# Performance work log

Hardware: AMD Instinct MI355X
Metric: run time of the kernel (lower is better)

Reference implementation:

```python
import jax, jax.numpy as jnp
import numpy as np

EPS = 1e-6


def _att_vector(x, W, b, sharp2, th2, is_last):
    """AttentionVector on a 2D payoff slice.
    x: (N, a, m). W: (1, 2), b: (1,). Returns (N, a)."""
    # compare_param: pair (x[n,j,k], x[n,i,k]) -> Linear(2,1) -> sigmoid -> mean over k
    # Linear on the concat pair is w00*x[n,j,k] + w01*x[n,i,k] + b, so we fuse it.
    lin = W[0, 0] * x[:, None, :, :] + W[0, 1] * x[:, :, None, :] + b[0]  # (N,a,a,m)
    c = jnp.mean(jax.nn.sigmoid(lin), axis=3)  # (N,a,a)
    # max_normalize over dim 2
    c = c / (jnp.max(c, axis=2, keepdims=True) + EPS)
    # compute_player_mask
    m = jnp.mean(c, axis=2)  # (N,a)
    m = jax.nn.relu(m * sharp2[0] + th2[0])
    m = jax.nn.softmax(m, axis=1)
    if not is_last:
        m = m / (jnp.max(m, axis=1, keepdims=True) + EPS)
    return m


def setup_inputs() -> dict:
    key = jax.random.key(0)
    ks = jax.random.split(key, 16)
    N, a1, a2, f = 128, 64, 64, 2
    inp = {
        "x": jax.random.normal(ks[0], (N, f, a1, a2), dtype=jnp.float32),
        "fc_W": jax.random.normal(ks[1], (2, 2), dtype=jnp.float32) * 0.5,
        "fc_b": jax.random.normal(ks[2], (2,), dtype=jnp.float32) * 0.1,
        "p1_W": jax.random.normal(ks[3], (1, 2), dtype=jnp.float32) * 0.5,
        "p1_b": jax.random.normal(ks[4], (1,), dtype=jnp.float32) * 0.1,
        "p1_sharp": jnp.ones((1,), dtype=jnp.float32),
        "p1_th": jnp.zeros((1,), dtype=jnp.float32),
        "p2_W": jax.random.normal(ks[5], (1, 2), dtype=jnp.float32) * 0.5,
        "p2_b": jax.random.normal(ks[6], (1,), dtype=jnp.float32) * 0.1,
        "p2_sharp": jnp.ones((1,), dtype=jnp.float32),
        "p2_th": jnp.zeros((1,), dtype=jnp.float32),
        "out_W": jax.random.normal(ks[7], (1, 2), dtype=jnp.float32) * 0.5,
        "out_b": jax.random.normal(ks[8], (1,), dtype=jnp.float32) * 0.1,
        "out_sharp": jnp.ones((1,), dtype=jnp.float32),
        "out_th": jnp.zeros((1,), dtype=jnp.float32),
    }
    return inp


def reference(x, fc_W, fc_b, p1_W, p1_b, p1_sharp, p1_th,
              p2_W, p2_b, p2_sharp, p2_th,
              out_W, out_b, out_sharp, out_th):
    # x: (N, f=2, a1, a2) -> (N, a1, a2, f)
    h = jnp.transpose(x, (0, 2, 3, 1))
    # is_fc_first: Linear(2, 2) + ReLU on last dim
    h = jax.nn.relu(h @ fc_W.T + fc_b)  # (N,a1,a2,2)
    # one AttentionModule (module_layers=1, not simult)
    vec1 = _att_vector(h[..., 0], p1_W, p1_b, p1_sharp, p1_th, is_last=False)  # (N,a1)
    h = h * vec1[:, :, None, None]
    pl2 = jnp.transpose(h[..., 1], (0, 2, 1))  # (N,a2,a1)
    vec2 = _att_vector(pl2, p2_W, p2_b, p2_sharp, p2_th, is_last=False)  # (N,a2)
    h = h * vec2[:, None, :, None]
    # with_last: final AttentionVector (is_last=True) on player-1 channel
    out = _att_vector(h[..., 0], out_W, out_b, out_sharp, out_th, is_last=True)  # (N,a1)
    return out
```

## Files before the change

kernel.cpp:

```cpp
#include <hip/hip_runtime.h>


constexpr int A   = 64;
constexpr int PAD = 65;
constexpr float L2E  = 1.4426950408889634f;
constexpr float EPSF = 1e-6f;

__device__ __forceinline__ float bcast(float v, int srcLane) {
    return __int_as_float(__builtin_amdgcn_readlane(__float_as_int(v), srcLane));
}
__device__ __forceinline__ float rcpf(float v) { return __builtin_amdgcn_rcpf(v); }
__device__ __forceinline__ float ex2(float v)  { return __builtin_amdgcn_exp2f(v); }

__device__ __forceinline__ void att2(const float* __restrict__ prow,
                                     const float* __restrict__ qrow,
                                     int row0, int lane,
                                     float* __restrict__ gm)
{
    float acc0 = 0.f, acc1 = 0.f;
#pragma unroll 1
    for (int c = 0; c < 4; ++c) {
        float pk[16], qk[16];
#pragma unroll
        for (int t = 0; t < 16; ++t) {
            pk[t] = prow[c * 16 + t];
            qk[t] = qrow[c * 16 + t];
        }
#pragma unroll
        for (int t = 0; t < 16; ++t) {
            float q0 = bcast(qk[t], row0);
            float q1 = bcast(qk[t], row0 + 1);
            acc0 += rcpf(fmaf(pk[t], q0, 1.0f));
            acc1 += rcpf(fmaf(pk[t], q1, 1.0f));
        }
    }
    float s0 = acc0, m0 = acc0, s1 = acc1, m1v = acc1;
#pragma unroll
    for (int off = 1; off < 64; off <<= 1) {
        s0 += __shfl_xor(s0, off, 64);
        m0 = fmaxf(m0, __shfl_xor(m0, off, 64));
        s1 += __shfl_xor(s1, off, 64);
        m1v = fmaxf(m1v, __shfl_xor(m1v, off, 64));
    }
    if (lane == 0) {
        gm[row0]     = (s0 * (1.0f / 4096.0f)) / (m0 * (1.0f / 64.0f) + EPSF);
        gm[row0 + 1] = (s1 * (1.0f / 4096.0f)) / (m1v * (1.0f / 64.0f) + EPSF);
    }
}

__device__ __forceinline__ float softmax64(float m, float sharp, float th, bool last)
{
    float v = fmaxf(0.f, m * sharp + th);
    float mx = v;
#pragma unroll
    for (int off = 1; off < 64; off <<= 1) mx = fmaxf(mx, __shfl_xor(mx, off, 64));
    float e = __expf(v - mx);
    float s = e;
#pragma unroll
    for (int off = 1; off < 64; off <<= 1) s += __shfl_xor(s, off, 64);
    float r = e / s;
    if (!last) {
        float rm = r;
#pragma unroll
        for (int off = 1; off < 64; off <<= 1) rm = fmaxf(rm, __shfl_xor(rm, off, 64));
        r = r / (rm + EPSF);
    }
    return r;
}

__global__ __launch_bounds__(1024, 1)
void k_stageB(const float* __restrict__ x,
              const float* __restrict__ fcW, const float* __restrict__ fcb,
              const float* __restrict__ p1W, const float* __restrict__ p1b,
              float* __restrict__ m1)
{
    __shared__ float pL[A * PAD];
    __shared__ float qL[A * PAD];
    const int tid = threadIdx.x, lane = tid & 63, wv = tid >> 6;
    const int n = blockIdx.x >> 1, half = blockIdx.x & 1;

    const float4* x0v = (const float4*)(x + (size_t)n * 2 * A * A);
    const float4* x1v = x0v + (A * A / 4);
    float4 a = x0v[tid];
    float4 c = x1v[tid];
    const float w00 = fcW[0], w01 = fcW[1], b0 = fcb[0];
    const float W0 = p1W[0], W1 = p1W[1], bb = p1b[0];
    const int e = tid * 4, i = e >> 6, j = e & 63;
    float hv[4] = { fmaxf(0.f, w00 * a.x + w01 * c.x + b0),
                    fmaxf(0.f, w00 * a.y + w01 * c.y + b0),
                    fmaxf(0.f, w00 * a.z + w01 * c.z + b0),
                    fmaxf(0.f, w00 * a.w + w01 * c.w + b0) };
#pragma unroll
    for (int t = 0; t < 4; ++t) {
        pL[i * PAD + j + t] = ex2(-L2E * (W0 * hv[t] + bb));
        qL[i * PAD + j + t] = ex2(-L2E * (W1 * hv[t]));
    }
    __syncthreads();

    const int row0 = half * 32 + wv * 2;
    att2(pL + lane * PAD, qL + lane * PAD, row0, lane, m1 + (size_t)n * A);
}

__global__ __launch_bounds__(1024, 1)
void k_stageC(const float* __restrict__ x,
              const float* __restrict__ fcW, const float* __restrict__ fcb,
              const float* __restrict__ p1s, const float* __restrict__ p1t,
              const float* __restrict__ p2W, const float* __restrict__ p2b,
              const float* __restrict__ m1, float* __restrict__ m2)
{
    __shared__ float pL[A * PAD];
    __shared__ float qL[A * PAD];
    __shared__ float v1buf[A];
    const int tid = threadIdx.x, lane = tid & 63, wv = tid >> 6;
    const int n = blockIdx.x >> 1, half = blockIdx.x & 1;

    const float4* x0v = (const float4*)(x + (size_t)n * 2 * A * A);
    const float4* x1v = x0v + (A * A / 4);
    float4 a = x0v[tid];
    float4 c = x1v[tid];

    if (tid < 64) v1buf[tid] = softmax64(m1[(size_t)n * A + tid], p1s[0], p1t[0], false);
    __syncthreads();

    const float w10 = fcW[2], w11 = fcW[3], b1 = fcb[1];
    const float W0 = p2W[0], W1 = p2W[1], bb = p2b[0];
    const int e = tid * 4, i = e >> 6, j = e & 63;
    const float sc = v1buf[i];
    float hv[4] = { fmaxf(0.f, w10 * a.x + w11 * c.x + b1) * sc,
                    fmaxf(0.f, w10 * a.y + w11 * c.y + b1) * sc,
                    fmaxf(0.f, w10 * a.z + w11 * c.z + b1) * sc,
                    fmaxf(0.f, w10 * a.w + w11 * c.w + b1) * sc };
#pragma unroll
    for (int t = 0; t < 4; ++t) {
        pL[(j + t) * PAD + i] = ex2(-L2E * (W0 * hv[t] + bb));
        qL[(j + t) * PAD + i] = ex2(-L2E * (W1 * hv[t]));
    }
    __syncthreads();

    const int row0 = half * 32 + wv * 2;
    att2(pL + lane * PAD, qL + lane * PAD, row0, lane, m2 + (size_t)n * A);
}

__global__ __launch_bounds__(1024, 1)
void k_stageD(const float* __restrict__ x,
              const float* __restrict__ fcW, const float* __restrict__ fcb,
              const float* __restrict__ p1s, const float* __restrict__ p1t,
              const float* __restrict__ p2s, const float* __restrict__ p2t,
              const float* __restrict__ oW,  const float* __restrict__ ob,
              const float* __restrict__ m1,  const float* __restrict__ m2,
              float* __restrict__ m3)
{
    __shared__ float pL[A * PAD];
    __shared__ float qL[A * PAD];
    __shared__ float v1buf[A], v2buf[A];
    const int tid = threadIdx.x, lane = tid & 63, wv = tid >> 6;
    const int n = blockIdx.x >> 1, half = blockIdx.x & 1;

    const float4* x0v = (const float4*)(x + (size_t)n * 2 * A * A);
    const float4* x1v = x0v + (A * A / 4);
    float4 a = x0v[tid];
    float4 c = x1v[tid];

    if (tid < 64)       v1buf[tid]      = softmax64(m1[(size_t)n * A + tid],      p1s[0], p1t[0], false);
    else if (tid < 128) v2buf[tid - 64] = softmax64(m2[(size_t)n * A + tid - 64], p2s[0], p2t[0], false);
    __syncthreads();

    const float w00 = fcW[0], w01 = fcW[1], b0 = fcb[0];
    const float W0 = oW[0], W1 = oW[1], bb = ob[0];
    const int e = tid * 4, i = e >> 6, j = e & 63;
    const float sc = v1buf[i];
    float hv[4] = { fmaxf(0.f, w00 * a.x + w01 * c.x + b0) * sc * v2buf[j],
                    fmaxf(0.f, w00 * a.y + w01 * c.y + b0) * sc * v2buf[j + 1],
                    fmaxf(0.f, w00 * a.z + w01 * c.z + b0) * sc * v2buf[j + 2],
                    fmaxf(0.f, w00 * a.w + w01 * c.w + b0) * sc * v2buf[j + 3] };
#pragma unroll
    for (int t = 0; t < 4; ++t) {
        pL[i * PAD + j + t] = ex2(-L2E * (W0 * hv[t] + bb));
        qL[i * PAD + j + t] = ex2(-L2E * (W1 * hv[t]));
    }
    __syncthreads();

    const int row0 = half * 32 + wv * 2;
    att2(pL + lane * PAD, qL + lane * PAD, row0, lane, m3 + (size_t)n * A);
}

__global__ __launch_bounds__(64, 1)
void k_final(const float* __restrict__ m3,
             const float* __restrict__ os, const float* __restrict__ ot,
             float* __restrict__ out)
{
    const int n = blockIdx.x, lane = threadIdx.x;
    out[(size_t)n * A + lane] = softmax64(m3[(size_t)n * A + lane], os[0], ot[0], true);
}

extern "C" void kernel_launch(void* const* d_in, const int* in_sizes, int n_in,
                              void* d_out, int out_size, void* d_ws, size_t ws_size,
                              hipStream_t stream)
{
    (void)n_in; (void)out_size; (void)ws_size;
    const float* x   = (const float*)d_in[0];
    const float* fcW = (const float*)d_in[1];
    const float* fcb = (const float*)d_in[2];
    const float* p1W = (const float*)d_in[3];
    const float* p1b = (const float*)d_in[4];
    const float* p1s = (const float*)d_in[5];
    const float* p1t = (const float*)d_in[6];
    const float* p2W = (const float*)d_in[7];
    const float* p2b = (const float*)d_in[8];
    const float* p2s = (const float*)d_in[9];
    const float* p2t = (const float*)d_in[10];
    const float* oW  = (const float*)d_in[11];
    const float* ob  = (const float*)d_in[12];
    const float* os  = (const float*)d_in[13];
    const float* ot  = (const float*)d_in[14];
    float* out = (float*)d_out;

    const int N = in_sizes[0] / (2 * A * A);
    float* ws = (float*)d_ws;
    float* m1 = ws;
    float* m2 = ws + (size_t)N * A;
    float* m3 = ws + (size_t)2 * N * A;

    k_stageB<<<2 * N, 1024, 0, stream>>>(x, fcW, fcb, p1W, p1b, m1);
    k_stageC<<<2 * N, 1024, 0, stream>>>(x, fcW, fcb, p1s, p1t, p2W, p2b, m1, m2);
    k_stageD<<<2 * N, 1024, 0, stream>>>(x, fcW, fcb, p1s, p1t, p2s, p2t, oW, ob, m1, m2, m3);
    k_final<<<N, 64, 0, stream>>>(m3, os, ot, out);
}
```

Before: 112.7 us.

## Fuse all attention stages into one per-sample kernel with 4-row accumulation

Replaces the three stage kernels and the final softmax kernel with a single kernel that runs one 1024-thread block per sample. The per-stage row vectors now stay in shared memory instead of a global workspace, and x is loaded once rather than three times. The pairwise sigmoid reduction now processes four rows per wave instead of two, for more instruction-level parallelism. In exchange the grid shrinks from 2N to N blocks, so half as many blocks cover the GPU and each does twice the work. The launch bound of 4 blocks per CU may also force a tight register cap.

```diff
diff --git a/kernel.cpp b/kernel.cpp
--- a/kernel.cpp
+++ b/kernel.cpp
@@ -12,12 +12,11 @@
 __device__ __forceinline__ float rcpf(float v) { return __builtin_amdgcn_rcpf(v); }
 __device__ __forceinline__ float ex2(float v)  { return __builtin_amdgcn_exp2f(v); }
 
-__device__ __forceinline__ void att2(const float* __restrict__ prow,
+__device__ __forceinline__ void att4(const float* __restrict__ prow,
                                      const float* __restrict__ qrow,
-                                     int row0, int lane,
-                                     float* __restrict__ gm)
+                                     int row0, int lane, float* __restrict__ mbuf)
 {
-    float acc0 = 0.f, acc1 = 0.f;
+    float acc0 = 0.f, acc1 = 0.f, acc2 = 0.f, acc3 = 0.f;
 #pragma unroll 1
     for (int c = 0; c < 4; ++c) {
         float pk[16], qk[16];
@@ -30,21 +29,28 @@
         for (int t = 0; t < 16; ++t) {
             float q0 = bcast(qk[t], row0);
             float q1 = bcast(qk[t], row0 + 1);
+            float q2 = bcast(qk[t], row0 + 2);
+            float q3 = bcast(qk[t], row0 + 3);
             acc0 += rcpf(fmaf(pk[t], q0, 1.0f));
             acc1 += rcpf(fmaf(pk[t], q1, 1.0f));
+            acc2 += rcpf(fmaf(pk[t], q2, 1.0f));
+            acc3 += rcpf(fmaf(pk[t], q3, 1.0f));
         }
     }
-    float s0 = acc0, m0 = acc0, s1 = acc1, m1v = acc1;
+    float s[4] = {acc0, acc1, acc2, acc3};
+    float m[4] = {acc0, acc1, acc2, acc3};
 #pragma unroll
     for (int off = 1; off < 64; off <<= 1) {
-        s0 += __shfl_xor(s0, off, 64);
-        m0 = fmaxf(m0, __shfl_xor(m0, off, 64));
-        s1 += __shfl_xor(s1, off, 64);
-        m1v = fmaxf(m1v, __shfl_xor(m1v, off, 64));
+#pragma unroll
+        for (int r = 0; r < 4; ++r) {
+            s[r] += __shfl_xor(s[r], off, 64);
+            m[r] = fmaxf(m[r], __shfl_xor(m[r], off, 64));
+        }
     }
     if (lane == 0) {
-        gm[row0]     = (s0 * (1.0f / 4096.0f)) / (m0 * (1.0f / 64.0f) + EPSF);
-        gm[row0 + 1] = (s1 * (1.0f / 4096.0f)) / (m1v * (1.0f / 64.0f) + EPSF);
+#pragma unroll
+        for (int r = 0; r < 4; ++r)
+            mbuf[row0 + r] = (s[r] * (1.0f / 4096.0f)) / (m[r] * (1.0f / 64.0f) + EPSF);
     }
 }
 
@@ -68,136 +74,98 @@
     return r;
 }
 
-__global__ __launch_bounds__(1024, 1)
-void k_stageB(const float* __restrict__ x,
-              const float* __restrict__ fcW, const float* __restrict__ fcb,
-              const float* __restrict__ p1W, const float* __restrict__ p1b,
-              float* __restrict__ m1)
+__global__ __launch_bounds__(1024, 4)
+void attn_fused(const float* __restrict__ x,
+                const float* __restrict__ fcW, const float* __restrict__ fcb,
+                const float* __restrict__ p1W, const float* __restrict__ p1b,
+                const float* __restrict__ p1s, const float* __restrict__ p1t,
+                const float* __restrict__ p2W, const float* __restrict__ p2b,
+                const float* __restrict__ p2s, const float* __restrict__ p2t,
+                const float* __restrict__ oW,  const float* __restrict__ ob,
+                const float* __restrict__ os,  const float* __restrict__ ot,
+                float* __restrict__ out)
 {
     __shared__ float pL[A * PAD];
     __shared__ float qL[A * PAD];
+    __shared__ float mbuf[A];
+    __shared__ float v1buf[A], v2buf[A];
+
     const int tid = threadIdx.x, lane = tid & 63, wv = tid >> 6;
-    const int n = blockIdx.x >> 1, half = blockIdx.x & 1;
+    const int n = blockIdx.x;
+    const int row0 = wv * 4;
+    const int i = tid >> 4, j = (tid & 15) * 4;
 
     const float4* x0v = (const float4*)(x + (size_t)n * 2 * A * A);
     const float4* x1v = x0v + (A * A / 4);
-    float4 a = x0v[tid];
-    float4 c = x1v[tid];
-    const float w00 = fcW[0], w01 = fcW[1], b0 = fcb[0];
-    const float W0 = p1W[0], W1 = p1W[1], bb = p1b[0];
-    const int e = tid * 4, i = e >> 6, j = e & 63;
-    float hv[4] = { fmaxf(0.f, w00 * a.x + w01 * c.x + b0),
-                    fmaxf(0.f, w00 * a.y + w01 * c.y + b0),
-                    fmaxf(0.f, w00 * a.z + w01 * c.z + b0),
-                    fmaxf(0.f, w00 * a.w + w01 * c.w + b0) };
+    const float4 a = x0v[tid];
+    const float4 c = x1v[tid];
+    const float w00 = fcW[0], w01 = fcW[1], w10 = fcW[2], w11 = fcW[3];
+    const float b0 = fcb[0], b1 = fcb[1];
+
+    const float h0v[4] = { fmaxf(0.f, w00 * a.x + w01 * c.x + b0),
+                           fmaxf(0.f, w00 * a.y + w01 * c.y + b0),
+                           fmaxf(0.f, w00 * a.z + w01 * c.z + b0),
+                           fmaxf(0.f, w00 * a.w + w01 * c.w + b0) };
+    const float h1v[4] = { fmaxf(0.f, w10 * a.x + w11 * c.x + b1),
+                           fmaxf(0.f, w10 * a.y + w11 * c.y + b1),
+                           fmaxf(0.f, w10 * a.z + w11 * c.z + b1),
+                           fmaxf(0.f, w10 * a.w + w11 * c.w + b1) };
+
+    {
+        const float W0 = p1W[0], W1 = p1W[1], bb = p1b[0];
 #pragma unroll
-    for (int t = 0; t < 4; ++t) {
-        pL[i * PAD + j + t] = ex2(-L2E * (W0 * hv[t] + bb));
-        qL[i * PAD + j + t] = ex2(-L2E * (W1 * hv[t]));
+        for (int t = 0; t < 4; ++t) {
+            pL[i * PAD + j + t] = ex2(-L2E * (W0 * h0v[t] + bb));
+            qL[i * PAD + j + t] = ex2(-L2E * (W1 * h0v[t]));
+        }
     }
     __syncthreads();
-
-    const int row0 = half * 32 + wv * 2;
-    att2(pL + lane * PAD, qL + lane * PAD, row0, lane, m1 + (size_t)n * A);
-}
-
-__global__ __launch_bounds__(1024, 1)
-void k_stageC(const float* __restrict__ x,
-              const float* __restrict__ fcW, const float* __restrict__ fcb,
-              const float* __restrict__ p1s, const float* __restrict__ p1t,
-              const float* __restrict__ p2W, const float* __restrict__ p2b,
-              const float* __restrict__ m1, float* __restrict__ m2)
-{
-    __shared__ float pL[A * PAD];
-    __shared__ float qL[A * PAD];
-    __shared__ float v1buf[A];
-    const int tid = threadIdx.x, lane = tid & 63, wv = tid >> 6;
-    const int n = blockIdx.x >> 1, half = blockIdx.x & 1;
-
-    const float4* x0v = (const float4*)(x + (size_t)n * 2 * A * A);
-    const float4* x1v = x0v + (A * A / 4);
-    float4 a = x0v[tid];
-    float4 c = x1v[tid];
-
-    if (tid < 64) v1buf[tid] = softmax64(m1[(size_t)n * A + tid], p1s[0], p1t[0], false);
+    att4(pL + lane * PAD, qL + lane * PAD, row0, lane, mbuf);
+    __syncthreads();
+    if (wv == 0) v1buf[lane] = softmax64(mbuf[lane], p1s[0], p1t[0], false);
     __syncthreads();
 
-    const float w10 = fcW[2], w11 = fcW[3], b1 = fcb[1];
-    const float W0 = p2W[0], W1 = p2W[1], bb = p2b[0];
-    const int e = tid * 4, i = e >> 6, j = e & 63;
-    const float sc = v1buf[i];
-    float hv[4] = { fmaxf(0.f, w10 * a.x + w11 * c.x + b1) * sc,
-                    fmaxf(0.f, w10 * a.y + w11 * c.y + b1) * sc,
-                    fmaxf(0.f, w10 * a.z + w11 * c.z + b1) * sc,
-                    fmaxf(0.f, w10 * a.w + w11 * c.w + b1) * sc };
+    {
+        const float W0 = p2W[0], W1 = p2W[1], bb = p2b[0];
+        const float sc = v1buf[i];
 #pragma unroll
-    for (int t = 0; t < 4; ++t) {
-        pL[(j + t) * PAD + i] = ex2(-L2E * (W0 * hv[t] + bb));
-        qL[(j + t) * PAD + i] = ex2(-L2E * (W1 * hv[t]));
+        for (int t = 0; t < 4; ++t) {
+            float hv = h1v[t] * sc;
+            pL[(j + t) * PAD + i] = ex2(-L2E * (W0 * hv + bb));
+            qL[(j + t) * PAD + i] = ex2(-L2E * (W1 * hv));
+        }
     }
     __syncthreads();
-
-    const int row0 = half * 32 + wv * 2;
-    att2(pL + lane * PAD, qL + lane * PAD, row0, lane, m2 + (size_t)n * A);
-}
-
-__global__ __launch_bounds__(1024, 1)
-void k_stageD(const float* __restrict__ x,
-              const float* __restrict__ fcW, const float* __restrict__ fcb,
-              const float* __restrict__ p1s, const float* __restrict__ p1t,
-              const float* __restrict__ p2s, const float* __restrict__ p2t,
-              const float* __restrict__ oW,  const float* __restrict__ ob,
-              const float* __restrict__ m1,  const float* __restrict__ m2,
-              float* __restrict__ m3)
-{
-    __shared__ float pL[A * PAD];
-    __shared__ float qL[A * PAD];
-    __shared__ float v1buf[A], v2buf[A];
-    const int tid = threadIdx.x, lane = tid & 63, wv = tid >> 6;
-    const int n = blockIdx.x >> 1, half = blockIdx.x & 1;
-
-    const float4* x0v = (const float4*)(x + (size_t)n * 2 * A * A);
-    const float4* x1v = x0v + (A * A / 4);
-    float4 a = x0v[tid];
-    float4 c = x1v[tid];
-
-    if (tid < 64)       v1buf[tid]      = softmax64(m1[(size_t)n * A + tid],      p1s[0], p1t[0], false);
-    else if (tid < 128) v2buf[tid - 64] = softmax64(m2[(size_t)n * A + tid - 64], p2s[0], p2t[0], false);
+    att4(pL + lane * PAD, qL + lane * PAD, row0, lane, mbuf);
+    __syncthreads();
+    if (wv == 0) v2buf[lane] = softmax64(mbuf[lane], p2s[0], p2t[0], false);
     __syncthreads();
 
-    const float w00 = fcW[0], w01 = fcW[1], b0 = fcb[0];
-    const float W0 = oW[0], W1 = oW[1], bb = ob[0];
-    const int e = tid * 4, i = e >> 6, j = e & 63;
-    const float sc = v1buf[i];
-    float hv[4] = { fmaxf(0.f, w00 * a.x + w01 * c.x + b0) * sc * v2buf[j],
-                    fmaxf(0.f, w00 * a.y + w01 * c.y + b0) * sc * v2buf[j + 1],
-                    fmaxf(0.f, w00 * a.z + w01 * c.z + b0) * sc * v2buf[j + 2],
-                    fmaxf(0.f, w00 * a.w + w01 * c.w + b0) * sc * v2buf[j + 3] };
+    {
+        const float W0 = oW[0], W1 = oW[1], bb = ob[0];
+        const float sc = v1buf[i];
+        const float4 v2q = *(const float4*)&v2buf[j];
+        const float v2a[4] = { v2q.x, v2q.y, v2q.z, v2q.w };
 #pragma unroll
-    for (int t = 0; t < 4; ++t) {
-        pL[i * PAD + j + t] = ex2(-L2E * (W0 * hv[t] + bb));
-        qL[i * PAD + j + t] = ex2(-L2E * (W1 * hv[t]));
+        for (int t = 0; t < 4; ++t) {
+            float hv = h0v[t] * sc * v2a[t];
+            pL[i * PAD + j + t] = ex2(-L2E * (W0 * hv + bb));
+            qL[i * PAD + j + t] = ex2(-L2E * (W1 * hv));
+        }
     }
     __syncthreads();
+    att4(pL + lane * PAD, qL + lane * PAD, row0, lane, mbuf);
+    __syncthreads();
 
-    const int row0 = half * 32 + wv * 2;
-    att2(pL + lane * PAD, qL + lane * PAD, row0, lane, m3 + (size_t)n * A);
-}
-
-__global__ __launch_bounds__(64, 1)
-void k_final(const float* __restrict__ m3,
-             const float* __restrict__ os, const float* __restrict__ ot,
-             float* __restrict__ out)
-{
-    const int n = blockIdx.x, lane = threadIdx.x;
-    out[(size_t)n * A + lane] = softmax64(m3[(size_t)n * A + lane], os[0], ot[0], true);
+    if (wv == 0)
+        out[(size_t)n * A + lane] = softmax64(mbuf[lane], os[0], ot[0], true);
 }
 
 extern "C" void kernel_launch(void* const* d_in, const int* in_sizes, int n_in,
                               void* d_out, int out_size, void* d_ws, size_t ws_size,
                               hipStream_t stream)
 {
-    (void)n_in; (void)out_size; (void)ws_size;
+    (void)n_in; (void)out_size; (void)d_ws; (void)ws_size;
     const float* x   = (const float*)d_in[0];
     const float* fcW = (const float*)d_in[1];
     const float* fcb = (const float*)d_in[2];
@@ -216,13 +184,8 @@
     float* out = (float*)d_out;
 
     const int N = in_sizes[0] / (2 * A * A);
-    float* ws = (float*)d_ws;
-    float* m1 = ws;
-    float* m2 = ws + (size_t)N * A;
-    float* m3 = ws + (size_t)2 * N * A;
-
-    k_stageB<<<2 * N, 1024, 0, stream>>>(x, fcW, fcb, p1W, p1b, m1);
-    k_stageC<<<2 * N, 1024, 0, stream>>>(x, fcW, fcb, p1s, p1t, p2W, p2b, m1, m2);
-    k_stageD<<<2 * N, 1024, 0, stream>>>(x, fcW, fcb, p1s, p1t, p2s, p2t, oW, ob, m1, m2, m3);
-    k_final<<<N, 64, 0, stream>>>(m3, os, ot, out);
+    attn_fused<<<N, 1024, 0, stream>>>(x, fcW, fcb,
+                                       p1W, p1b, p1s, p1t,
+                                       p2W, p2b, p2s, p2t,
+                                       oW, ob, os, ot, out);
 }
```

Measured after the change: 120.8 us. +7.2%, slower.
